# Optimization experiments

Hardware: AMD Instinct MI355X
Metric: run time of the kernel (lower is better)

## Reference

```python
import jax, jax.numpy as jnp
import numpy as np

B, T, D, H, G = 256, 1024, 32, 64, 4 * 64  # batch, seq, input, hidden, gates


def setup_inputs() -> dict:
    key = jax.random.key(0)
    ks = jax.random.split(key, 12)
    s = 1.0 / np.sqrt(H)  # PyTorch LSTM default init scale
    return {
        "x": jax.random.normal(ks[0], (B, T, D), dtype=jnp.float32),
        "w_ih_l0": jax.random.normal(ks[1], (G, D), dtype=jnp.float32) * s,
        "w_hh_l0": jax.random.normal(ks[2], (G, H), dtype=jnp.float32) * s,
        "b_ih_l0": jax.random.normal(ks[3], (G,), dtype=jnp.float32) * s,
        "b_hh_l0": jax.random.normal(ks[4], (G,), dtype=jnp.float32) * s,
        "w_ih_l1": jax.random.normal(ks[5], (G, H), dtype=jnp.float32) * s,
        "w_hh_l1": jax.random.normal(ks[6], (G, H), dtype=jnp.float32) * s,
        "b_ih_l1": jax.random.normal(ks[7], (G,), dtype=jnp.float32) * s,
        "b_hh_l1": jax.random.normal(ks[8], (G,), dtype=jnp.float32) * s,
        "w_fc": jax.random.normal(ks[9], (1, H), dtype=jnp.float32) * s,
        "b_fc": jax.random.normal(ks[10], (1,), dtype=jnp.float32) * s,
    }


def _lstm_layer(x, w_ih, w_hh, b_ih, b_hh):
    """x: [B, T, Din] -> h_seq [B, T, H]. PyTorch gate order (i, f, g, o)."""
    # Precompute input contribution for all timesteps in one GEMM.
    gx = jnp.einsum('btd,gd->btg', x, w_ih) + b_ih + b_hh  # [B, T, 4H]
    gx = jnp.swapaxes(gx, 0, 1)  # [T, B, 4H] for scan over time
    h0 = jnp.zeros((x.shape[0], H), dtype=x.dtype)
    c0 = jnp.zeros((x.shape[0], H), dtype=x.dtype)

    def step(carry, g_t):
        h, c = carry
        g = g_t + h @ w_hh.T  # [B, 4H]
        i, f, gg, o = jnp.split(g, 4, axis=-1)
        i = jax.nn.sigmoid(i)
        f = jax.nn.sigmoid(f)
        gg = jnp.tanh(gg)
        o = jax.nn.sigmoid(o)
        c = f * c + i * gg
        h = o * jnp.tanh(c)
        return (h, c), h

    _, h_seq = jax.lax.scan(step, (h0, c0), gx)  # h_seq: [T, B, H]
    return jnp.swapaxes(h_seq, 0, 1)  # [B, T, H]


def reference(x, w_ih_l0, w_hh_l0, b_ih_l0, b_hh_l0,
              w_ih_l1, w_hh_l1, b_ih_l1, b_hh_l1, w_fc, b_fc):
    h1 = _lstm_layer(x, w_ih_l0, w_hh_l0, b_ih_l0, b_hh_l0)
    h2 = _lstm_layer(h1, w_ih_l1, w_hh_l1, b_ih_l1, b_hh_l1)
    last = h2[:, -1, :]  # [B, H]
    logits = last @ w_fc.T + b_fc  # [B, 1]
    return jax.nn.sigmoid(logits)
```

## Files before the change

### kernel.cpp

```cpp
#include <hip/hip_runtime.h>

#define TT 1024
#define DD 32
#define HH 64

typedef __fp16 h2v __attribute__((ext_vector_type(2)));
typedef _Float16 f16x8 __attribute__((ext_vector_type(8)));
typedef float f32x4 __attribute__((ext_vector_type(4)));

struct __attribute__((aligned(16))) H4 { h2v p[4]; };

__device__ __forceinline__ h2v pk(float a, float b) {
    return __builtin_amdgcn_cvt_pkrtz(a, b);
}
__device__ __forceinline__ float fsig(float x) {
    float e = __builtin_amdgcn_exp2f(-1.4426950408889634f * x);
    return __builtin_amdgcn_rcpf(1.0f + e);
}
__device__ __forceinline__ float ftanh(float x) {
    float e = __builtin_amdgcn_exp2f(2.885390081777927f * x);
    return 1.0f - 2.0f * __builtin_amdgcn_rcpf(1.0f + e);
}
__device__ __forceinline__ float pick4(f32x4 c, bool s0, bool s1) {
    float lo = s0 ? c[1] : c[0];
    float hi = s0 ? c[3] : c[2];
    return s1 ? hi : lo;
}
__device__ __forceinline__ f16x8 load_afrag(const float* p) {
    float4 f0 = *(const float4*)p;
    float4 f1 = *(const float4*)(p + 4);
    H4 t;
    t.p[0] = pk(f0.x, f0.y); t.p[1] = pk(f0.z, f0.w);
    t.p[2] = pk(f1.x, f1.y); t.p[3] = pk(f1.z, f1.w);
    return __builtin_bit_cast(f16x8, t);
}
#define MFMA16(A, B, C) __builtin_amdgcn_mfma_f32_16x16x32_f16(A, B, C, 0, 0, 0)

__global__ __launch_bounds__(512) void lstm2_b4(
    const float* __restrict__ x,
    const float* __restrict__ w_ih_l0, const float* __restrict__ w_hh_l0,
    const float* __restrict__ b_ih_l0, const float* __restrict__ b_hh_l0,
    const float* __restrict__ w_ih_l1, const float* __restrict__ w_hh_l1,
    const float* __restrict__ b_ih_l1, const float* __restrict__ b_hh_l1,
    const float* __restrict__ w_fc,   const float* __restrict__ b_fc,
    float* __restrict__ out)
{
    const int bbase = blockIdx.x * 4;
    const int tid  = threadIdx.x;
    const int wave = tid >> 6;
    const int lane = tid & 63;
    const bool isL1 = wave < 4;
    const int js   = wave & 3;
    const int quad = lane >> 4;
    const int bb   = lane & 3;
    const int rsel = (lane >> 2) & 3;
    const int jj   = js*16 + quad*4 + rsel;
    const int mrow = lane & 15;

    __shared__ __attribute__((aligned(16))) __fp16 buf[2560];

    {
        int* bi = (int*)buf;
        bi[tid] = 0;
        bi[512 + tid] = 0;
        if (tid < 256) bi[1024 + tid] = 0;
    }

    f16x8 A[16];
    f32x4 bv0, bv1, bv2, bv3;
    if (isL1) {
        #pragma unroll
        for (int q = 0; q < 4; ++q) {
            const int g = q*64 + js*16 + mrow;
            A[q*3 + 0] = load_afrag(w_ih_l0 + (size_t)g*DD + quad*8);
            A[q*3 + 1] = load_afrag(w_hh_l0 + (size_t)g*HH + quad*8);
            A[q*3 + 2] = load_afrag(w_hh_l0 + (size_t)g*HH + 32 + quad*8);
        }
        #pragma unroll
        for (int r = 0; r < 4; ++r) {
            const int j4 = js*16 + quad*4 + r;
            bv0[r] = b_ih_l0[0*64 + j4] + b_hh_l0[0*64 + j4];
            bv1[r] = b_ih_l0[1*64 + j4] + b_hh_l0[1*64 + j4];
            bv2[r] = b_ih_l0[2*64 + j4] + b_hh_l0[2*64 + j4];
            bv3[r] = b_ih_l0[3*64 + j4] + b_hh_l0[3*64 + j4];
        }
    } else {
        #pragma unroll
        for (int q = 0; q < 4; ++q) {
            const int g = q*64 + js*16 + mrow;
            A[q*4 + 0] = load_afrag(w_ih_l1 + (size_t)g*HH + quad*8);
            A[q*4 + 1] = load_afrag(w_ih_l1 + (size_t)g*HH + 32 + quad*8);
            A[q*4 + 2] = load_afrag(w_hh_l1 + (size_t)g*HH + quad*8);
            A[q*4 + 3] = load_afrag(w_hh_l1 + (size_t)g*HH + 32 + quad*8);
        }
        #pragma unroll
        for (int r = 0; r < 4; ++r) {
            const int j4 = js*16 + quad*4 + r;
            bv0[r] = b_ih_l1[0*64 + j4] + b_hh_l1[0*64 + j4];
            bv1[r] = b_ih_l1[1*64 + j4] + b_hh_l1[1*64 + j4];
            bv2[r] = b_ih_l1[2*64 + j4] + b_hh_l1[2*64 + j4];
            bv3[r] = b_ih_l1[3*64 + j4] + b_hh_l1[3*64 + j4];
        }
    }

    const int roff = (bb*4 + quad)*8;
    const int cw   = (isL1 ? 1 : 3) + (jj >> 5);
    const int woff = ((cw*4 + bb)*4 + ((jj & 31) >> 3))*8 + (jj & 7);

    const float* xg = x + (size_t)(bbase + (lane >> 4)) * (TT*DD) + (lane & 15)*2;
    const int sdw = ((lane >> 4)*4 + ((lane & 15) >> 2))*4 + ((lane & 15) & 3);
    float2 xv1 = {0.f, 0.f}, xv2 = {0.f, 0.f};

    __syncthreads();
    if (wave == 0) {
        float2 v0 = *(const float2*)xg;
        ((int*)(buf + 0*640))[sdw] = __builtin_bit_cast(int, pk(v0.x, v0.y));
        float2 v1 = *(const float2*)(xg + DD);
        ((int*)(buf + 1*640))[sdw] = __builtin_bit_cast(int, pk(v1.x, v1.y));
        xv1 = *(const float2*)(xg + 2*DD);
        xv2 = *(const float2*)(xg + 3*DD);
    }
    __syncthreads();

    f32x4 Ca0 = bv0, Ca1 = bv1, Ca2 = bv2, Ca3 = bv3;
    f32x4 Cb0 = bv0, Cb1 = bv1, Cb2 = bv2, Cb3 = bv3;
    if (isL1) {
        f16x8 B0 = *(const f16x8*)(buf + 0*640 + roff);
        Ca0 = MFMA16(A[0], B0, bv0);
        Ca1 = MFMA16(A[3], B0, bv1);
        Ca2 = MFMA16(A[6], B0, bv2);
        Ca3 = MFMA16(A[9], B0, bv3);
    }

    const bool s0 = (rsel & 1) != 0;
    const bool s1 = (rsel & 2) != 0;
    float cst = 0.0f;

#define ACT_WRITE(SLOT, C0_, C1_, C2_, C3_)                                   \
    {   float Si = pick4(C0_, s0, s1);                 \
        float Sf = pick4(C1_, s0, s1);                                        \
        float Sg = pick4(C2_, s0, s1);                                        \
        float So = pick4(C3_, s0, s1);                                        \
        float ii = fsig(Si), ff = fsig(Sf), oo = fsig(So);                    \
        float gg = ftanh(Sg);                                                 \
        cst = ff * cst + ii * gg;                                             \
        float hv = oo * ftanh(cst);                                           \
        buf[(SLOT)*640 + woff] = (__fp16)hv;                                  \
    }

#define STEP(K, P0,P1,P2,P3, Q0,Q1,Q2,Q3)                                     \
    {   const int t = tb + (K);                                               \
        if (wave == 0 && (t + 2 < TT)) {      \
            ((int*)(buf + (((K)+2)&3)*640))[sdw] =                            \
                __builtin_bit_cast(int, pk(xv1.x, xv1.y));                    \
            xv1 = xv2;                                                        \
            const int tl = (t + 4 < TT) ? (t + 4) : (TT - 1);                 \
            xv2 = *(const float2*)(xg + (size_t)tl*DD);                       \
        }                                                                     \
        if (isL1) {                                                           \
            if (t < TT) {                     \
                const __fp16* bp = buf + (((K)-1)&3)*640;                     \
                f16x8 B1 = *(const f16x8*)(bp + 128 + roff);                  \
                f16x8 B2 = *(const f16x8*)(bp + 256 + roff);                  \
                P0 = MFMA16(A[1],  B1, P0); P0 = MFMA16(A[2],  B2, P0);       \
                P1 = MFMA16(A[4],  B1, P1); P1 = MFMA16(A[5],  B2, P1);       \
                P2 = MFMA16(A[7],  B1, P2); P2 = MFMA16(A[8],  B2, P2);       \
                P3 = MFMA16(A[10], B1, P3); P3 = MFMA16(A[11], B2, P3);       \
                ACT_WRITE((K)&3, P0, P1, P2, P3);                             \
            }                                                                 \
            if (t < TT - 1) {                    \
                f16x8 B0 = *(const f16x8*)(buf + (((K)+1)&3)*640 + roff);     \
                Q0 = MFMA16(A[0], B0, bv0);                                   \
                Q1 = MFMA16(A[3], B0, bv1);                                   \
                Q2 = MFMA16(A[6], B0, bv2);                                   \
                Q3 = MFMA16(A[9], B0, bv3);                                   \
            }                                                                 \
        } else {                                                              \
            if (t >= 2 && t <= TT + 1) {      \
                const __fp16* bp = buf + (((K)-3)&3)*640;                     \
                f16x8 B3 = *(const f16x8*)(bp + 384 + roff);                  \
                f16x8 B4 = *(const f16x8*)(bp + 512 + roff);                  \
                P0 = MFMA16(A[2],  B3, P0); P0 = MFMA16(A[3],  B4, P0);       \
                P1 = MFMA16(A[6],  B3, P1); P1 = MFMA16(A[7],  B4, P1);       \
                P2 = MFMA16(A[10], B3, P2); P2 = MFMA16(A[11], B4, P2);       \
                P3 = MFMA16(A[14], B3, P3); P3 = MFMA16(A[15], B4, P3);       \
                ACT_WRITE(((K)-2)&3, P0, P1, P2, P3);            \
            }                                                                 \
            if (t >= 1 && t <= TT) {            \
                const __fp16* bp = buf + (((K)-1)&3)*640;                     \
                f16x8 B1 = *(const f16x8*)(bp + 128 + roff);                  \
                f16x8 B2 = *(const f16x8*)(bp + 256 + roff);                  \
                Q0 = MFMA16(A[0],  B1, bv0); Q0 = MFMA16(A[1],  B2, Q0);      \
                Q1 = MFMA16(A[4],  B1, bv1); Q1 = MFMA16(A[5],  B2, Q1);      \
                Q2 = MFMA16(A[8],  B1, bv2); Q2 = MFMA16(A[9],  B2, Q2);      \
                Q3 = MFMA16(A[12], B1, bv3); Q3 = MFMA16(A[13], B2, Q3);      \
            }                                                                 \
        }                                                                     \
        __syncthreads();                                                      \
    }

    for (int tb = 0; tb < TT + 4; tb += 4) {
        STEP(0, Ca0,Ca1,Ca2,Ca3, Cb0,Cb1,Cb2,Cb3)
        STEP(1, Cb0,Cb1,Cb2,Cb3, Ca0,Ca1,Ca2,Ca3)
        STEP(2, Ca0,Ca1,Ca2,Ca3, Cb0,Cb1,Cb2,Cb3)
        STEP(3, Cb0,Cb1,Cb2,Cb3, Ca0,Ca1,Ca2,Ca3)
    }

#undef STEP
#undef ACT_WRITE

    if (wave == 0) {
        const int jg = lane >> 2;
        float s = 0.f;
        #pragma unroll
        for (int u2 = 0; u2 < 4; ++u2) {
            const int j = jg*4 + u2;
            float hval = (float)buf[3*640 +
                (((3 + (j >> 5))*4 + bb)*4 + ((j & 31) >> 3))*8 + (j & 7)];
            s += hval * w_fc[j];
        }
        s += __shfl_xor(s, 4);
        s += __shfl_xor(s, 8);
        s += __shfl_xor(s, 16);
        s += __shfl_xor(s, 32);
        if (lane < 4) out[bbase + lane] = fsig(s + b_fc[0]);
    }
}

extern "C" void kernel_launch(void* const* d_in, const int* in_sizes, int n_in,
                              void* d_out, int out_size, void* d_ws, size_t ws_size,
                              hipStream_t stream) {
    lstm2_b4<<<dim3(64), dim3(512), 0, stream>>>(
        (const float*)d_in[0],
        (const float*)d_in[1], (const float*)d_in[2],
        (const float*)d_in[3], (const float*)d_in[4],
        (const float*)d_in[5], (const float*)d_in[6],
        (const float*)d_in[7], (const float*)d_in[8],
        (const float*)d_in[9], (const float*)d_in[10],
        (float*)d_out);
}
```

Before: 561.9 us.

## Split LSTM layers into separate producer/consumer blocks synced via global flags

Layer 1 and layer 2 now run in separate workgroups (128 blocks of 256 threads instead of 64 blocks of 512). They pass h1 through a global fp16 buffer, with release/acquire progress counters polled every 8 steps. The aim is to cut each block's per-step barrier cost and spread the work over more CUs, since each block now syncs only four waves. In exchange, layer 2 depends on global-memory latency and spin-waiting, and it relies on all 128 blocks being co-resident, or it could deadlock.

```diff
diff --git a/kernel.cpp b/kernel.cpp
--- a/kernel.cpp
+++ b/kernel.cpp
@@ -7,8 +7,10 @@
 typedef __fp16 h2v __attribute__((ext_vector_type(2)));
 typedef _Float16 f16x8 __attribute__((ext_vector_type(8)));
 typedef float f32x4 __attribute__((ext_vector_type(4)));
+typedef unsigned long long u64;
 
 struct __attribute__((aligned(16))) H4 { h2v p[4]; };
+struct __attribute__((aligned(16))) U2 { u64 a, b; };
 
 __device__ __forceinline__ h2v pk(float a, float b) {
     return __builtin_amdgcn_cvt_pkrtz(a, b);
@@ -34,41 +36,55 @@
     t.p[2] = pk(f1.x, f1.y); t.p[3] = pk(f1.z, f1.w);
     return __builtin_bit_cast(f16x8, t);
 }
+__device__ __forceinline__ f16x8 mkfrag(u64 lo, u64 hi) {
+    U2 t{lo, hi};
+    return __builtin_bit_cast(f16x8, t);
+}
+__device__ __forceinline__ u64 gld(const __fp16* p) {
+    return __hip_atomic_load((const u64*)p, __ATOMIC_RELAXED,
+                             __HIP_MEMORY_SCOPE_AGENT);
+}
 #define MFMA16(A, B, C) __builtin_amdgcn_mfma_f32_16x16x32_f16(A, B, C, 0, 0, 0)
 
-__global__ __launch_bounds__(512) void lstm2_b4(
+__global__ __launch_bounds__(256) void lstm2_split(
     const float* __restrict__ x,
     const float* __restrict__ w_ih_l0, const float* __restrict__ w_hh_l0,
     const float* __restrict__ b_ih_l0, const float* __restrict__ b_hh_l0,
     const float* __restrict__ w_ih_l1, const float* __restrict__ w_hh_l1,
     const float* __restrict__ b_ih_l1, const float* __restrict__ b_hh_l1,
     const float* __restrict__ w_fc,   const float* __restrict__ b_fc,
-    float* __restrict__ out)
+    float* __restrict__ out,
+    int* __restrict__ prog, __fp16* __restrict__ h1g)
 {
-    const int bbase = blockIdx.x * 4;
+    const int role = blockIdx.x >> 6;
+    const int grp  = blockIdx.x & 63;
+    const int bbase = grp * 4;
     const int tid  = threadIdx.x;
     const int wave = tid >> 6;
     const int lane = tid & 63;
-    const bool isL1 = wave < 4;
-    const int js   = wave & 3;
+    const int js   = wave;
     const int quad = lane >> 4;
     const int bb   = lane & 3;
     const int rsel = (lane >> 2) & 3;
     const int jj   = js*16 + quad*4 + rsel;
     const int mrow = lane & 15;
-
-    __shared__ __attribute__((aligned(16))) __fp16 buf[2560];
+    const bool s0 = (rsel & 1) != 0;
+    const bool s1 = (rsel & 2) != 0;
+    const int roff = (bb*4 + quad)*8;
+
+    __shared__ __attribute__((aligned(16))) __fp16 buf[1536];
 
     {
         int* bi = (int*)buf;
-        bi[tid] = 0;
-        bi[512 + tid] = 0;
-        if (tid < 256) bi[1024 + tid] = 0;
+        bi[tid] = 0; bi[256 + tid] = 0; bi[512 + tid] = 0;
     }
-
-    f16x8 A[16];
-    f32x4 bv0, bv1, bv2, bv3;
-    if (isL1) {
+    __syncthreads();
+
+    float cst = 0.0f;
+
+    if (role == 0) {
+        f16x8 A[12];
+        f32x4 bv0, bv1, bv2, bv3;
         #pragma unroll
         for (int q = 0; q < 4; ++q) {
             const int g = q*64 + js*16 + mrow;
@@ -84,7 +100,95 @@
             bv2[r] = b_ih_l0[2*64 + j4] + b_hh_l0[2*64 + j4];
             bv3[r] = b_ih_l0[3*64 + j4] + b_hh_l0[3*64 + j4];
         }
+        const int whoff = 128 + (((jj>>5)*4 + bb)*4 + ((jj&31)>>3))*8 + (jj&7);
+        const bool do_st = ((rsel & 1) == 0);
+        const int gdw = ((jj>>5)*4 + bb)*16 + ((jj&31)>>3)*4 + ((jj&7)>>1);
+        unsigned int* h1gw = (unsigned int*)h1g + grp*128 + gdw;
+
+        const float* xg = x + (size_t)(bbase + (lane >> 4))*(TT*DD) + (lane & 15)*2;
+        const int sdw = ((lane>>4)*4 + ((lane&15)>>2))*4 + ((lane&15)&3);
+        float2 xv1 = {0.f, 0.f}, xv2 = {0.f, 0.f};
+
+        if (wave == 0) {
+            float2 v0 = *(const float2*)xg;
+            ((int*)(buf + 0*384))[sdw] = __builtin_bit_cast(int, pk(v0.x, v0.y));
+            float2 v1 = *(const float2*)(xg + DD);
+            ((int*)(buf + 1*384))[sdw] = __builtin_bit_cast(int, pk(v1.x, v1.y));
+            xv1 = *(const float2*)(xg + 2*DD);
+            xv2 = *(const float2*)(xg + 3*DD);
+        }
+        __syncthreads();
+
+        f32x4 Ca0, Ca1, Ca2, Ca3, Cb0, Cb1, Cb2, Cb3;
+        {
+            f16x8 B0 = *(const f16x8*)(buf + 0*384 + roff);
+            Ca0 = MFMA16(A[0], B0, bv0);
+            Ca1 = MFMA16(A[3], B0, bv1);
+            Ca2 = MFMA16(A[6], B0, bv2);
+            Ca3 = MFMA16(A[9], B0, bv3);
+            Cb0 = bv0; Cb1 = bv1; Cb2 = bv2; Cb3 = bv3;
+        }
+
+#define L1STEP(K, P0,P1,P2,P3, Q0,Q1,Q2,Q3)                                   \
+    {   const int t = tb + (K);                                               \
+        if (tid == 0 && (t & 7) == 0 && t)                                    \
+            __hip_atomic_store(prog + grp, t, __ATOMIC_RELEASE,               \
+                               __HIP_MEMORY_SCOPE_AGENT);                     \
+        if (wave == 0 && (t + 2 < TT)) {                                      \
+            ((int*)(buf + (((K)+2)&3)*384))[sdw] =                            \
+                __builtin_bit_cast(int, pk(xv1.x, xv1.y));                    \
+            xv1 = xv2;                                                        \
+            const int tl = (t + 4 < TT) ? (t + 4) : (TT - 1);                 \
+            xv2 = *(const float2*)(xg + (size_t)tl*DD);                       \
+        }                                                                     \
+        {   const __fp16* bp = buf + (((K)-1)&3)*384;                         \
+            f16x8 B1 = *(const f16x8*)(bp + 128 + roff);                      \
+            f16x8 B2 = *(const f16x8*)(bp + 256 + roff);                      \
+            P0 = MFMA16(A[1],  B1, P0); P0 = MFMA16(A[2],  B2, P0);           \
+            P1 = MFMA16(A[4],  B1, P1); P1 = MFMA16(A[5],  B2, P1);           \
+            P2 = MFMA16(A[7],  B1, P2); P2 = MFMA16(A[8],  B2, P2);           \
+            P3 = MFMA16(A[10], B1, P3); P3 = MFMA16(A[11], B2, P3);           \
+            float Si = pick4(P0, s0, s1);                                     \
+            float Sf = pick4(P1, s0, s1);                                     \
+            float Sg = pick4(P2, s0, s1);                                     \
+            float So = pick4(P3, s0, s1);                                     \
+            float ii = fsig(Si), ff = fsig(Sf), oo = fsig(So);                \
+            float gg = ftanh(Sg);                                             \
+            cst = ff * cst + ii * gg;                                         \
+            float hv = oo * ftanh(cst);                                       \
+            __fp16 hh_ = (__fp16)hv;                                          \
+            buf[((K)&3)*384 + whoff] = hh_;                                   \
+            unsigned int us = (unsigned int)__builtin_bit_cast(               \
+                                  unsigned short, hh_);                       \
+            unsigned int pu = (unsigned int)__shfl_xor((int)us, 4);           \
+            if (do_st)                                                        \
+                __hip_atomic_store(h1gw + (size_t)t*8192,                     \
+                                   us | (pu << 16), __ATOMIC_RELAXED,         \
+                                   __HIP_MEMORY_SCOPE_AGENT);                 \
+        }                                                                     \
+        if (t < TT - 1) {                                                     \
+            f16x8 B0 = *(const f16x8*)(buf + (((K)+1)&3)*384 + roff);         \
+            Q0 = MFMA16(A[0], B0, bv0);                                       \
+            Q1 = MFMA16(A[3], B0, bv1);                                       \
+            Q2 = MFMA16(A[6], B0, bv2);                                       \
+            Q3 = MFMA16(A[9], B0, bv3);                                       \
+        }                                                                     \
+        __syncthreads();                                                      \
+    }
+
+        for (int tb = 0; tb < TT; tb += 4) {
+            L1STEP(0, Ca0,Ca1,Ca2,Ca3, Cb0,Cb1,Cb2,Cb3)
+            L1STEP(1, Cb0,Cb1,Cb2,Cb3, Ca0,Ca1,Ca2,Ca3)
+            L1STEP(2, Ca0,Ca1,Ca2,Ca3, Cb0,Cb1,Cb2,Cb3)
+            L1STEP(3, Cb0,Cb1,Cb2,Cb3, Ca0,Ca1,Ca2,Ca3)
+        }
+#undef L1STEP
+        if (tid == 0)
+            __hip_atomic_store(prog + grp, TT, __ATOMIC_RELEASE,
+                               __HIP_MEMORY_SCOPE_AGENT);
     } else {
+        f16x8 A[16];
+        f32x4 bv0, bv1, bv2, bv3;
         #pragma unroll
         for (int q = 0; q < 4; ++q) {
             const int g = q*64 + js*16 + mrow;
@@ -101,141 +205,99 @@
             bv2[r] = b_ih_l1[2*64 + j4] + b_hh_l1[2*64 + j4];
             bv3[r] = b_ih_l1[3*64 + j4] + b_hh_l1[3*64 + j4];
         }
-    }
-
-    const int roff = (bb*4 + quad)*8;
-    const int cw   = (isL1 ? 1 : 3) + (jj >> 5);
-    const int woff = ((cw*4 + bb)*4 + ((jj & 31) >> 3))*8 + (jj & 7);
-
-    const float* xg = x + (size_t)(bbase + (lane >> 4)) * (TT*DD) + (lane & 15)*2;
-    const int sdw = ((lane >> 4)*4 + ((lane & 15) >> 2))*4 + ((lane & 15) & 3);
-    float2 xv1 = {0.f, 0.f}, xv2 = {0.f, 0.f};
-
-    __syncthreads();
-    if (wave == 0) {
-        float2 v0 = *(const float2*)xg;
-        ((int*)(buf + 0*640))[sdw] = __builtin_bit_cast(int, pk(v0.x, v0.y));
-        float2 v1 = *(const float2*)(xg + DD);
-        ((int*)(buf + 1*640))[sdw] = __builtin_bit_cast(int, pk(v1.x, v1.y));
-        xv1 = *(const float2*)(xg + 2*DD);
-        xv2 = *(const float2*)(xg + 3*DD);
-    }
-    __syncthreads();
-
-    f32x4 Ca0 = bv0, Ca1 = bv1, Ca2 = bv2, Ca3 = bv3;
-    f32x4 Cb0 = bv0, Cb1 = bv1, Cb2 = bv2, Cb3 = bv3;
-    if (isL1) {
-        f16x8 B0 = *(const f16x8*)(buf + 0*640 + roff);
-        Ca0 = MFMA16(A[0], B0, bv0);
-        Ca1 = MFMA16(A[3], B0, bv1);
-        Ca2 = MFMA16(A[6], B0, bv2);
-        Ca3 = MFMA16(A[9], B0, bv3);
-    }
-
-    const bool s0 = (rsel & 1) != 0;
-    const bool s1 = (rsel & 2) != 0;
-    float cst = 0.0f;
-
-#define ACT_WRITE(SLOT, C0_, C1_, C2_, C3_)                                   \
-    {   float Si = pick4(C0_, s0, s1);                 \
-        float Sf = pick4(C1_, s0, s1);                                        \
-        float Sg = pick4(C2_, s0, s1);                                        \
-        float So = pick4(C3_, s0, s1);                                        \
+        const int whoff2 = (((jj>>5)*4 + bb)*4 + ((jj&31)>>3))*8 + (jj&7);
+        const __fp16* h1r = h1g + grp*256 + roff;
+
+        {   const int need = 12;
+            while (__hip_atomic_load(prog + grp, __ATOMIC_ACQUIRE,
+                                     __HIP_MEMORY_SCOPE_AGENT) < need)
+                __builtin_amdgcn_s_sleep(4);
+        }
+        u64 g0a, g0b, g0c, g0d, g1a = 0, g1b = 0, g1c = 0, g1d = 0;
+        {   const __fp16* gp = h1r;
+            g0a = gld(gp);       g0b = gld(gp + 4);
+            g0c = gld(gp + 128); g0d = gld(gp + 132);
+        }
+
+#define L2STEP(K, Ga_,Gb_,Gc_,Gd_, Pa_,Pb_,Pc_,Pd_)                           \
+    {   const int t = tb + (K);                                               \
+        if ((t & 7) == 0 && t) {                                              \
+            const int need = (t + 12 < TT) ? (t + 12) : TT;                   \
+            while (__hip_atomic_load(prog + grp, __ATOMIC_ACQUIRE,            \
+                                     __HIP_MEMORY_SCOPE_AGENT) < need)        \
+                __builtin_amdgcn_s_sleep(4);                                  \
+        }                                                                     \
+        if (t + 1 < TT) {           \
+            const __fp16* gp = h1r + (size_t)(t + 1)*16384;                   \
+            Pa_ = gld(gp);       Pb_ = gld(gp + 4);                           \
+            Pc_ = gld(gp + 128); Pd_ = gld(gp + 132);                         \
+        }                                                                     \
+        f16x8 B1 = mkfrag(Ga_, Gb_);                                          \
+        f16x8 B2 = mkfrag(Gc_, Gd_);                                          \
+        f32x4 C0, C1, C2, C3;                                                 \
+        C0 = MFMA16(A[0],  B1, bv0); C0 = MFMA16(A[1],  B2, C0);              \
+        C1 = MFMA16(A[4],  B1, bv1); C1 = MFMA16(A[5],  B2, C1);              \
+        C2 = MFMA16(A[8],  B1, bv2); C2 = MFMA16(A[9],  B2, C2);              \
+        C3 = MFMA16(A[12], B1, bv3); C3 = MFMA16(A[13], B2, C3);              \
+        {   const __fp16* bp = buf + (((K)-1)&3)*256;                         \
+            f16x8 D3 = *(const f16x8*)(bp + roff);                            \
+            f16x8 D4 = *(const f16x8*)(bp + 128 + roff);                      \
+            C0 = MFMA16(A[2],  D3, C0); C0 = MFMA16(A[3],  D4, C0);           \
+            C1 = MFMA16(A[6],  D3, C1); C1 = MFMA16(A[7],  D4, C1);           \
+            C2 = MFMA16(A[10], D3, C2); C2 = MFMA16(A[11], D4, C2);           \
+            C3 = MFMA16(A[14], D3, C3); C3 = MFMA16(A[15], D4, C3);           \
+        }                                                                     \
+        float Si = pick4(C0, s0, s1);                                         \
+        float Sf = pick4(C1, s0, s1);                                         \
+        float Sg = pick4(C2, s0, s1);                                         \
+        float So = pick4(C3, s0, s1);                                         \
         float ii = fsig(Si), ff = fsig(Sf), oo = fsig(So);                    \
         float gg = ftanh(Sg);                                                 \
         cst = ff * cst + ii * gg;                                             \
         float hv = oo * ftanh(cst);                                           \
-        buf[(SLOT)*640 + woff] = (__fp16)hv;                                  \
-    }
-
-#define STEP(K, P0,P1,P2,P3, Q0,Q1,Q2,Q3)                                     \
-    {   const int t = tb + (K);                                               \
-        if (wave == 0 && (t + 2 < TT)) {      \
-            ((int*)(buf + (((K)+2)&3)*640))[sdw] =                            \
-                __builtin_bit_cast(int, pk(xv1.x, xv1.y));                    \
-            xv1 = xv2;                                                        \
-            const int tl = (t + 4 < TT) ? (t + 4) : (TT - 1);                 \
-            xv2 = *(const float2*)(xg + (size_t)tl*DD);                       \
-        }                                                                     \
-        if (isL1) {                                                           \
-            if (t < TT) {                     \
-                const __fp16* bp = buf + (((K)-1)&3)*640;                     \
-                f16x8 B1 = *(const f16x8*)(bp + 128 + roff);                  \
-                f16x8 B2 = *(const f16x8*)(bp + 256 + roff);                  \
-                P0 = MFMA16(A[1],  B1, P0); P0 = MFMA16(A[2],  B2, P0);       \
-                P1 = MFMA16(A[4],  B1, P1); P1 = MFMA16(A[5],  B2, P1);       \
-                P2 = MFMA16(A[7],  B1, P2); P2 = MFMA16(A[8],  B2, P2);       \
-                P3 = MFMA16(A[10], B1, P3); P3 = MFMA16(A[11], B2, P3);       \
-                ACT_WRITE((K)&3, P0, P1, P2, P3);                             \
-            }                                                                 \
-            if (t < TT - 1) {                    \
-                f16x8 B0 = *(const f16x8*)(buf + (((K)+1)&3)*640 + roff);     \
-                Q0 = MFMA16(A[0], B0, bv0);                                   \
-                Q1 = MFMA16(A[3], B0, bv1);                                   \
-                Q2 = MFMA16(A[6], B0, bv2);                                   \
-                Q3 = MFMA16(A[9], B0, bv3);                                   \
-            }                                                                 \
-        } else {                                                              \
-            if (t >= 2 && t <= TT + 1) {      \
-                const __fp16* bp = buf + (((K)-3)&3)*640;                     \
-                f16x8 B3 = *(const f16x8*)(bp + 384 + roff);                  \
-                f16x8 B4 = *(const f16x8*)(bp + 512 + roff);                  \
-                P0 = MFMA16(A[2],  B3, P0); P0 = MFMA16(A[3],  B4, P0);       \
-                P1 = MFMA16(A[6],  B3, P1); P1 = MFMA16(A[7],  B4, P1);       \
-                P2 = MFMA16(A[10], B3, P2); P2 = MFMA16(A[11], B4, P2);       \
-                P3 = MFMA16(A[14], B3, P3); P3 = MFMA16(A[15], B4, P3);       \
-                ACT_WRITE(((K)-2)&3, P0, P1, P2, P3);            \
-            }                                                                 \
-            if (t >= 1 && t <= TT) {            \
-                const __fp16* bp = buf + (((K)-1)&3)*640;                     \
-                f16x8 B1 = *(const f16x8*)(bp + 128 + roff);                  \
-                f16x8 B2 = *(const f16x8*)(bp + 256 + roff);                  \
-                Q0 = MFMA16(A[0],  B1, bv0); Q0 = MFMA16(A[1],  B2, Q0);      \
-                Q1 = MFMA16(A[4],  B1, bv1); Q1 = MFMA16(A[5],  B2, Q1);      \
-                Q2 = MFMA16(A[8],  B1, bv2); Q2 = MFMA16(A[9],  B2, Q2);      \
-                Q3 = MFMA16(A[12], B1, bv3); Q3 = MFMA16(A[13], B2, Q3);      \
-            }                                                                 \
-        }                                                                     \
+        buf[((K)&3)*256 + whoff2] = (__fp16)hv;                               \
         __syncthreads();                                                      \
     }
 
-    for (int tb = 0; tb < TT + 4; tb += 4) {
-        STEP(0, Ca0,Ca1,Ca2,Ca3, Cb0,Cb1,Cb2,Cb3)
-        STEP(1, Cb0,Cb1,Cb2,Cb3, Ca0,Ca1,Ca2,Ca3)
-        STEP(2, Ca0,Ca1,Ca2,Ca3, Cb0,Cb1,Cb2,Cb3)
-        STEP(3, Cb0,Cb1,Cb2,Cb3, Ca0,Ca1,Ca2,Ca3)
-    }
-
-#undef STEP
-#undef ACT_WRITE
-
-    if (wave == 0) {
-        const int jg = lane >> 2;
-        float s = 0.f;
-        #pragma unroll
-        for (int u2 = 0; u2 < 4; ++u2) {
-            const int j = jg*4 + u2;
-            float hval = (float)buf[3*640 +
-                (((3 + (j >> 5))*4 + bb)*4 + ((j & 31) >> 3))*8 + (j & 7)];
-            s += hval * w_fc[j];
-        }
-        s += __shfl_xor(s, 4);
-        s += __shfl_xor(s, 8);
-        s += __shfl_xor(s, 16);
-        s += __shfl_xor(s, 32);
-        if (lane < 4) out[bbase + lane] = fsig(s + b_fc[0]);
+        for (int tb = 0; tb < TT; tb += 4) {
+            L2STEP(0, g0a,g0b,g0c,g0d, g1a,g1b,g1c,g1d)
+            L2STEP(1, g1a,g1b,g1c,g1d, g0a,g0b,g0c,g0d)
+            L2STEP(2, g0a,g0b,g0c,g0d, g1a,g1b,g1c,g1d)
+            L2STEP(3, g1a,g1b,g1c,g1d, g0a,g0b,g0c,g0d)
+        }
+#undef L2STEP
+
+        if (wave == 0) {
+            const int jg = lane >> 2;
+            float s = 0.f;
+            #pragma unroll
+            for (int u2 = 0; u2 < 4; ++u2) {
+                const int j = jg*4 + u2;
+                float hval = (float)buf[3*256 +
+                    (((j>>5)*4 + bb)*4 + ((j&31)>>3))*8 + (j&7)];
+                s += hval * w_fc[j];
+            }
+            s += __shfl_xor(s, 4);
+            s += __shfl_xor(s, 8);
+            s += __shfl_xor(s, 16);
+            s += __shfl_xor(s, 32);
+            if (lane < 4) out[bbase + lane] = fsig(s + b_fc[0]);
+        }
     }
 }
 
 extern "C" void kernel_launch(void* const* d_in, const int* in_sizes, int n_in,
                               void* d_out, int out_size, void* d_ws, size_t ws_size,
                               hipStream_t stream) {
-    lstm2_b4<<<dim3(64), dim3(512), 0, stream>>>(
+    int* prog = (int*)d_ws;
+    __fp16* h1g = (__fp16*)((char*)d_ws + 256);
+    hipMemsetAsync(d_ws, 0, 256, stream);
+    lstm2_split<<<dim3(128), dim3(256), 0, stream>>>(
         (const float*)d_in[0],
         (const float*)d_in[1], (const float*)d_in[2],
         (const float*)d_in[3], (const float*)d_in[4],
         (const float*)d_in[5], (const float*)d_in[6],
         (const float*)d_in[7], (const float*)d_in[8],
         (const float*)d_in[9], (const float*)d_in[10],
-        (float*)d_out);
-}
+        (float*)d_out, prog, h1g);
+}
```

Result: slower. 782.4 us (+39.2%).
